# Performance work log

Hardware: AMD Instinct MI355X
Metric: run time of the kernel (lower is better)

## Reference

```python
import jax, jax.numpy as jnp
import numpy as np

EMBED_DIM = 1024
NUM_HEADS = 16
HEAD_DIM = EMBED_DIM // NUM_HEADS


def setup_inputs() -> dict:
    key = jax.random.key(0)
    ks = jax.random.split(key, 9)
    B, T, C = 2, 2048, EMBED_DIM
    s = 1.0 / np.sqrt(C)
    return {
        "x": jax.random.normal(ks[0], (B, T, C), dtype=jnp.float32),
        "Wq": jax.random.normal(ks[1], (C, C), dtype=jnp.float32) * s,
        "bq": jnp.zeros((C,), dtype=jnp.float32),
        "Wk": jax.random.normal(ks[2], (C, C), dtype=jnp.float32) * s,
        "bk": jnp.zeros((C,), dtype=jnp.float32),
        "Wv": jax.random.normal(ks[3], (C, C), dtype=jnp.float32) * s,
        "bv": jnp.zeros((C,), dtype=jnp.float32),
        "Wo": jax.random.normal(ks[4], (C, C), dtype=jnp.float32) * s,
        "bo": jnp.zeros((C,), dtype=jnp.float32),
    }


def reference(x, Wq, bq, Wk, bk, Wv, bv, Wo, bo):
    B, T, C = x.shape
    H, D = NUM_HEADS, HEAD_DIM
    # projections (torch Linear: x @ W.T + b; here W stored as [in,out])
    q = (x @ Wq + bq).reshape(B, T, H, D).transpose(0, 2, 1, 3)  # [B,H,T,D]
    k = (x @ Wk + bk).reshape(B, T, H, D).transpose(0, 2, 1, 3)
    v = (x @ Wv + bv).reshape(B, T, H, D).transpose(0, 2, 1, 3)
    scores = jnp.einsum("bhtd,bhsd->bhts", q, k) / jnp.sqrt(jnp.float32(D))
    causal = jnp.tril(jnp.ones((T, T), dtype=bool))  # keep lower triangle
    scores = jnp.where(causal, scores, -jnp.inf)
    weights = jax.nn.softmax(scores, axis=-1)
    attended = jnp.einsum("bhts,bhsd->bhtd", weights, v)
    attended = attended.transpose(0, 2, 1, 3).reshape(B, T, C)
    return attended @ Wo + bo
```

## Files before the change

kernel.cpp:

```cpp
#include <hip/hip_runtime.h>
#include <math.h>


#define BLOCK 256

typedef __attribute__((ext_vector_type(8))) short bf16x8;
typedef __attribute__((ext_vector_type(4))) float f32x4;
typedef __attribute__((ext_vector_type(16))) float f32x16;

__device__ inline short f2bf(float f) {
  union { float f; unsigned u; } c; c.f = f;
  unsigned u = c.u;
  unsigned r = (u + 0x7fffu + ((u >> 16) & 1u)) >> 16;
  return (short)r;
}

#define GLD_LDS16(g, l)                                            \
  __builtin_amdgcn_global_load_lds(                                \
      (const __attribute__((address_space(1))) unsigned int*)(g),  \
      (__attribute__((address_space(3))) unsigned int*)(l), 16, 0, 0)


__global__ void cvt_x_kernel(const float* __restrict__ x, short* __restrict__ xb) {
  int i = (blockIdx.x * BLOCK + threadIdx.x) * 8;
  float4 a = *(const float4*)(x + i);
  float4 b = *(const float4*)(x + i + 4);
  alignas(16) short o[8];
  o[0] = f2bf(a.x); o[1] = f2bf(a.y); o[2] = f2bf(a.z); o[3] = f2bf(a.w);
  o[4] = f2bf(b.x); o[5] = f2bf(b.y); o[6] = f2bf(b.z); o[7] = f2bf(b.w);
  *(int4*)(xb + i) = *(int4*)o;
}

__global__ void cvt_w_kernel(const float* __restrict__ Wq, const float* __restrict__ Wk,
                             const float* __restrict__ Wv, const float* __restrict__ Wo,
                             short* __restrict__ Wtqkv, short* __restrict__ Wto) {
  __shared__ float tile[32][33];
  int z = blockIdx.z;
  const float* W = (z == 0) ? Wq : (z == 1) ? Wk : (z == 2) ? Wv : Wo;
  short* outp = (z == 3) ? Wto : (Wtqkv + (size_t)z * 1024 * 1024);
  int k0 = blockIdx.x * 32, n0 = blockIdx.y * 32;
  int tr = threadIdx.x >> 5, tc = threadIdx.x & 31;
#pragma unroll
  for (int i = 0; i < 4; i++)
    tile[tr + i * 8][tc] = W[(k0 + tr + i * 8) * 1024 + n0 + tc];
  __syncthreads();
#pragma unroll
  for (int i = 0; i < 4; i++)
    outp[(n0 + tr + i * 8) * 1024 + k0 + tc] = f2bf(tile[tc][tr + i * 8]);
}


__global__ __launch_bounds__(BLOCK) void gemm_qkv_kernel(
    const short* __restrict__ A, const short* __restrict__ Wt,
    const float* __restrict__ bq, const float* __restrict__ bk,
    const float* __restrict__ bv,
    short* __restrict__ Qo, short* __restrict__ Ko, short* __restrict__ Vo) {
  const int Kd = 1024;
  const float QSCL = 0.18033688011f;
  int m0 = blockIdx.x * 128, n0 = blockIdx.y * 128;
  int t = threadIdx.x;
  int lane = t & 63, wv = t >> 6;
  int quad = lane >> 4, lc = lane & 15;
  int wy = wv >> 1, wx = wv & 1;
  __shared__ short As[2][128 * 32];
  __shared__ short Bs[2][128 * 32];
  f32x4 acc[4][4] = {};
  int r0 = t >> 2, c0 = (t & 3) * 8;
  const short* Arow0 = A + (size_t)(m0 + r0) * Kd + c0;
  const short* Arow1 = A + (size_t)(m0 + r0 + 64) * Kd + c0;
  const short* Brow0 = Wt + (size_t)(n0 + r0) * Kd + c0;
  const short* Brow1 = Wt + (size_t)(n0 + r0 + 64) * Kd + c0;
  GLD_LDS16(Arow0, &As[0][8 * t]);
  GLD_LDS16(Arow1, &As[0][8 * t + 2048]);
  GLD_LDS16(Brow0, &Bs[0][8 * t]);
  GLD_LDS16(Brow1, &Bs[0][8 * t + 2048]);
  int cur = 0;
  for (int k0 = 0; k0 < Kd; k0 += 32) {
    __syncthreads();
    if (k0 + 32 < Kd) {
      int nxt = cur ^ 1;
      GLD_LDS16(Arow0 + k0 + 32, &As[nxt][8 * t]);
      GLD_LDS16(Arow1 + k0 + 32, &As[nxt][8 * t + 2048]);
      GLD_LDS16(Brow0 + k0 + 32, &Bs[nxt][8 * t]);
      GLD_LDS16(Brow1 + k0 + 32, &Bs[nxt][8 * t + 2048]);
    }
    bf16x8 af[4], bf[4];
#pragma unroll
    for (int i = 0; i < 4; i++)
      af[i] = *(const bf16x8*)&As[cur][(wy * 64 + i * 16 + lc) * 32 + quad * 8];
#pragma unroll
    for (int i = 0; i < 4; i++)
      bf[i] = *(const bf16x8*)&Bs[cur][(wx * 64 + i * 16 + lc) * 32 + quad * 8];
#pragma unroll
    for (int mi = 0; mi < 4; mi++)
#pragma unroll
      for (int ni = 0; ni < 4; ni++)
        acc[mi][ni] = __builtin_amdgcn_mfma_f32_16x16x32_bf16(af[mi], bf[ni], acc[mi][ni], 0, 0, 0);
    cur ^= 1;
  }
#pragma unroll
  for (int mi = 0; mi < 4; mi++) {
    int row = m0 + wy * 64 + mi * 16 + quad * 4;
#pragma unroll
    for (int ni = 0; ni < 4; ni++) {
      int col = n0 + wx * 64 + ni * 16 + lc;
      int which = col >> 10;
      int hd = col & 1023;
      int h = hd >> 6, d = hd & 63;
      float bb = (which == 0) ? bq[hd] : (which == 1) ? bk[hd] : bv[hd];
      if (which == 2) {
        alignas(8) short pk[4];
#pragma unroll
        for (int r = 0; r < 4; r++) pk[r] = f2bf(acc[mi][ni][r] + bb);
        int b = row >> 11, tt = row & 2047;
        *(int2*)&Vo[((size_t)(b * 16 + h) * 64 + d) * 2048 + tt] = *(const int2*)pk;
      } else {
#pragma unroll
        for (int r = 0; r < 4; r++) {
          int rw = row + r;
          int b = rw >> 11, tt = rw & 2047;
          float val = acc[mi][ni][r] + bb;
          if (which == 0) {
            Qo[((size_t)(b * 16 + h) * 2048 + tt) * 64 + d] = f2bf(val * QSCL);
          } else {
            Ko[((size_t)(b * 16 + h) * 2048 + tt) * 64 + d] = f2bf(val);
          }
        }
      }
    }
  }
}


__global__ __launch_bounds__(BLOCK) void gemm_out_kernel(
    const short* __restrict__ A, const short* __restrict__ Wt,
    const float* __restrict__ bias, float* __restrict__ Out) {
  const int Kd = 1024;
  int m0 = blockIdx.x * 64, n0 = blockIdx.y * 128;
  int t = threadIdx.x;
  int lane = t & 63, wv = t >> 6;
  int quad = lane >> 4, lc = lane & 15;
  int wy = wv >> 1, wx = wv & 1;
  __shared__ short As[64 * 32];
  __shared__ short Bs[128 * 32];
  int r0 = t >> 2, c0 = (t & 3) * 8;
  f32x4 acc[2][4] = {};
  const short* Arow0 = A + (size_t)(m0 + r0) * Kd + c0;
  const short* Brow0 = Wt + (size_t)(n0 + r0) * Kd + c0;
  const short* Brow1 = Wt + (size_t)(n0 + r0 + 64) * Kd + c0;
  for (int k0 = 0; k0 < Kd; k0 += 32) {
    __syncthreads();
    GLD_LDS16(Arow0 + k0, &As[8 * t]);
    GLD_LDS16(Brow0 + k0, &Bs[8 * t]);
    GLD_LDS16(Brow1 + k0, &Bs[8 * t + 2048]);
    __syncthreads();
    bf16x8 af[2], bf[4];
#pragma unroll
    for (int i = 0; i < 2; i++)
      af[i] = *(const bf16x8*)&As[(wy * 32 + i * 16 + lc) * 32 + quad * 8];
#pragma unroll
    for (int i = 0; i < 4; i++)
      bf[i] = *(const bf16x8*)&Bs[(wx * 64 + i * 16 + lc) * 32 + quad * 8];
#pragma unroll
    for (int mi = 0; mi < 2; mi++)
#pragma unroll
      for (int ni = 0; ni < 4; ni++)
        acc[mi][ni] = __builtin_amdgcn_mfma_f32_16x16x32_bf16(af[mi], bf[ni], acc[mi][ni], 0, 0, 0);
  }
#pragma unroll
  for (int mi = 0; mi < 2; mi++) {
    int row = m0 + wy * 32 + mi * 16 + quad * 4;
#pragma unroll
    for (int ni = 0; ni < 4; ni++) {
      int col = n0 + wx * 64 + ni * 16 + lc;
      float bb = bias[col];
#pragma unroll
      for (int r = 0; r < 4; r++)
        Out[(size_t)(row + r) * 1024 + col] = acc[mi][ni][r] + bb;
    }
  }
}


__global__ __launch_bounds__(BLOCK, 3) void attn_kernel(
    const short* __restrict__ Q, const short* __restrict__ K,
    const short* __restrict__ Vt, short* __restrict__ Oa) {
  int bh = blockIdx.x >> 4;
  int pair = blockIdx.x & 15;
  int t = threadIdx.x;
  int lane = t & 63, w = t >> 6;
  int qhalf = w & 1, par = w >> 1;
  int ln = lane & 31, lh = lane >> 5;
  const short* Qb = Q + (size_t)bh * 2048 * 64;
  const short* Kb = K + (size_t)bh * 2048 * 64;
  const short* Vg = Vt + (size_t)bh * 64 * 2048;
  int b = bh >> 4, h = bh & 15;

  __shared__ short Kt[64 * 72];
  __shared__ short Vs[64 * 72];
  __shared__ __align__(16) short Ps[4][32 * 72];
  __shared__ float lx[2][64];
  short* Pw = Ps[w];

  int srow = t >> 2;
  int scol = (t & 3) * 16;
  const float M2 = 14.5f;

  for (int sp = 0; sp < 2; sp++) {
    int s = sp ? (31 - pair) : pair;
    int q0 = s * 64;
    int q0w = q0 + qhalf * 32;
    int ntiles = s + 1;

    bf16x8 qf[4];
#pragma unroll
    for (int c = 0; c < 4; c++)
      qf[c] = *(const bf16x8*)&Qb[(size_t)(q0w + ln) * 64 + c * 16 + lh * 8];

    f32x16 O0 = {}, O1 = {};
    float lsum = 0.f;

    int4 ka0 = *(const int4*)&Kb[(size_t)srow * 64 + scol];
    int4 ka1 = *(const int4*)&Kb[(size_t)srow * 64 + scol + 8];
    int4 va0 = *(const int4*)&Vg[(size_t)srow * 2048 + scol];
    int4 va1 = *(const int4*)&Vg[(size_t)srow * 2048 + scol + 8];
    __syncthreads();
    *(int4*)&Kt[srow * 72 + scol] = ka0;
    *(int4*)&Kt[srow * 72 + scol + 8] = ka1;
    *(int4*)&Vs[srow * 72 + scol] = va0;
    *(int4*)&Vs[srow * 72 + scol + 8] = va1;
    __syncthreads();

    for (int kt = 0; kt < ntiles; kt++) {
      bool more = (kt + 1 < ntiles);
      if (more) {
        int kb2 = (kt + 1) * 64;
        ka0 = *(const int4*)&Kb[(size_t)(kb2 + srow) * 64 + scol];
        ka1 = *(const int4*)&Kb[(size_t)(kb2 + srow) * 64 + scol + 8];
        va0 = *(const int4*)&Vg[(size_t)srow * 2048 + kb2 + scol];
        va1 = *(const int4*)&Vg[(size_t)srow * 2048 + kb2 + scol + 8];
      }
      if ((kt & 1) == par) {
        int kbase = kt * 64;
        f32x16 S[2] = {};
#pragma unroll
        for (int c = 0; c < 4; c++) {
          bf16x8 k0 = *(const bf16x8*)&Kt[ln * 72 + c * 16 + lh * 8];
          bf16x8 k1 = *(const bf16x8*)&Kt[(32 + ln) * 72 + c * 16 + lh * 8];
          S[0] = __builtin_amdgcn_mfma_f32_32x32x16_bf16(k0, qf[c], S[0], 0, 0, 0);
          S[1] = __builtin_amdgcn_mfma_f32_32x32x16_bf16(k1, qf[c], S[1], 0, 0, 0);
        }
        if (kt == ntiles - 1) {
          int qg = q0w + ln;
#pragma unroll
          for (int kh = 0; kh < 2; kh++)
#pragma unroll
            for (int reg = 0; reg < 16; reg++) {
              int key = kbase + kh * 32 + (reg & 3) + 8 * (reg >> 2) + 4 * lh;
              if (key > qg) S[kh][reg] = -3.0e38f;
            }
        }
#pragma unroll
        for (int kh = 0; kh < 2; kh++)
#pragma unroll
          for (int g = 0; g < 4; g++) {
            unsigned u[4];
#pragma unroll
            for (int i = 0; i < 4; i++) {
              union { float f; unsigned v; } cc;
              cc.f = __builtin_amdgcn_exp2f(S[kh][g * 4 + i] - M2);
              lsum += cc.f;
              u[i] = cc.v + 0x8000u;
            }
            int2 pk;
            pk.x = (int)__builtin_amdgcn_perm(u[1], u[0], 0x07060302);
            pk.y = (int)__builtin_amdgcn_perm(u[3], u[2], 0x07060302);
            *(int2*)&Pw[ln * 72 + kh * 32 + g * 8 + lh * 4] = pk;
          }
#pragma unroll
        for (int c = 0; c < 4; c++) {
          bf16x8 pf = *(const bf16x8*)&Pw[ln * 72 + c * 16 + lh * 8];
          bf16x8 v0 = *(const bf16x8*)&Vs[ln * 72 + c * 16 + lh * 8];
          bf16x8 v1 = *(const bf16x8*)&Vs[(32 + ln) * 72 + c * 16 + lh * 8];
          O0 = __builtin_amdgcn_mfma_f32_32x32x16_bf16(v0, pf, O0, 0, 0, 0);
          O1 = __builtin_amdgcn_mfma_f32_32x32x16_bf16(v1, pf, O1, 0, 0, 0);
        }
      }
      if (more) {
        __syncthreads();
        *(int4*)&Kt[srow * 72 + scol] = ka0;
        *(int4*)&Kt[srow * 72 + scol + 8] = ka1;
        *(int4*)&Vs[srow * 72 + scol] = va0;
        *(int4*)&Vs[srow * 72 + scol + 8] = va1;
        __syncthreads();
      }
    }

    float* ob = (float*)&Ps[0][0];
    __syncthreads();
    if (par == 1) {
      float* obw = ob + qhalf * 2048;
#pragma unroll
      for (int dh = 0; dh < 2; dh++)
#pragma unroll
        for (int reg = 0; reg < 16; reg++)
          obw[((dh * 16 + reg) * 2 + lh) * 32 + ln] = dh ? O1[reg] : O0[reg];
      lx[qhalf][lane] = lsum;
    }
    __syncthreads();
    if (par == 0) {
      float* obw = ob + qhalf * 2048;
#pragma unroll
      for (int reg = 0; reg < 16; reg++) {
        O0[reg] += obw[((0 * 16 + reg) * 2 + lh) * 32 + ln];
        O1[reg] += obw[((1 * 16 + reg) * 2 + lh) * 32 + ln];
      }
      float lt = lsum + lx[qhalf][lane];
      lt += __shfl_xor(lt, 32, 64);
      float inv = 1.0f / lt;
      size_t rowbase = (size_t)(b * 2048 + q0w + ln) * 1024 + h * 64;
#pragma unroll
      for (int dh = 0; dh < 2; dh++)
#pragma unroll
        for (int g = 0; g < 4; g++) {
          alignas(8) short pk[4];
#pragma unroll
          for (int i = 0; i < 4; i++) {
            float v = dh ? O1[g * 4 + i] : O0[g * 4 + i];
            pk[i] = f2bf(v * inv);
          }
          *(int2*)&Oa[rowbase + dh * 32 + g * 8 + lh * 4] = *(const int2*)pk;
        }
    }
  }
}


extern "C" void kernel_launch(void* const* d_in, const int* in_sizes, int n_in,
                              void* d_out, int out_size, void* d_ws, size_t ws_size,
                              hipStream_t stream) {
  const float* x = (const float*)d_in[0];
  const float* Wq = (const float*)d_in[1];
  const float* bq = (const float*)d_in[2];
  const float* Wk = (const float*)d_in[3];
  const float* bk = (const float*)d_in[4];
  const float* Wv = (const float*)d_in[5];
  const float* bv = (const float*)d_in[6];
  const float* Wo = (const float*)d_in[7];
  const float* bo = (const float*)d_in[8];
  char* ws = (char*)d_ws;
  const size_t MB = 1024 * 1024;
  short* xb = (short*)(ws);
  short* Wtqkv = (short*)(ws + 8 * MB);
  short* Wto = (short*)(ws + 14 * MB);
  short* Qb = (short*)(ws + 17 * MB);
  short* Kb = (short*)(ws + 25 * MB);
  short* Vb = (short*)(ws + 33 * MB);
  short* Att = (short*)(ws + 41 * MB);
  float* out = (float*)d_out;

  cvt_x_kernel<<<2048, BLOCK, 0, stream>>>(x, xb);
  cvt_w_kernel<<<dim3(32, 32, 4), BLOCK, 0, stream>>>(Wq, Wk, Wv, Wo, Wtqkv, Wto);
  gemm_qkv_kernel<<<dim3(32, 24), BLOCK, 0, stream>>>(xb, Wtqkv, bq, bk, bv, Qb, Kb, Vb);
  attn_kernel<<<512, BLOCK, 0, stream>>>(Qb, Kb, Vb, Att);
  gemm_out_kernel<<<dim3(64, 8), BLOCK, 0, stream>>>(Att, Wto, bo, out);
}
```

Before: 193.5 us.

## Double-buffer output GEMM LDS and restructure attention into 128-key superstages

The output-projection GEMM now double-buffers its LDS tiles with direct global-to-LDS loads, prefetching the next K slice while computing the current one and dropping one barrier per iteration. The attention kernel stages 128 keys per iteration instead of 64 and splits key work between wave pairs by 32-key halves rather than alternating tiles. Key groups lying entirely above the causal diagonal are skipped, and fewer barriers run per key. This uses more LDS and registers, so launch bounds drop from 3 to 2 blocks per CU, which may reduce occupancy.

```diff
diff --git a/kernel.cpp b/kernel.cpp
--- a/kernel.cpp
+++ b/kernel.cpp
@@ -141,31 +141,38 @@
   int lane = t & 63, wv = t >> 6;
   int quad = lane >> 4, lc = lane & 15;
   int wy = wv >> 1, wx = wv & 1;
-  __shared__ short As[64 * 32];
-  __shared__ short Bs[128 * 32];
+  __shared__ short As[2][64 * 32];
+  __shared__ short Bs[2][128 * 32];
   int r0 = t >> 2, c0 = (t & 3) * 8;
   f32x4 acc[2][4] = {};
   const short* Arow0 = A + (size_t)(m0 + r0) * Kd + c0;
   const short* Brow0 = Wt + (size_t)(n0 + r0) * Kd + c0;
   const short* Brow1 = Wt + (size_t)(n0 + r0 + 64) * Kd + c0;
+  GLD_LDS16(Arow0, &As[0][8 * t]);
+  GLD_LDS16(Brow0, &Bs[0][8 * t]);
+  GLD_LDS16(Brow1, &Bs[0][8 * t + 2048]);
+  int cur = 0;
   for (int k0 = 0; k0 < Kd; k0 += 32) {
     __syncthreads();
-    GLD_LDS16(Arow0 + k0, &As[8 * t]);
-    GLD_LDS16(Brow0 + k0, &Bs[8 * t]);
-    GLD_LDS16(Brow1 + k0, &Bs[8 * t + 2048]);
-    __syncthreads();
+    if (k0 + 32 < Kd) {
+      int nxt = cur ^ 1;
+      GLD_LDS16(Arow0 + k0 + 32, &As[nxt][8 * t]);
+      GLD_LDS16(Brow0 + k0 + 32, &Bs[nxt][8 * t]);
+      GLD_LDS16(Brow1 + k0 + 32, &Bs[nxt][8 * t + 2048]);
+    }
     bf16x8 af[2], bf[4];
 #pragma unroll
     for (int i = 0; i < 2; i++)
-      af[i] = *(const bf16x8*)&As[(wy * 32 + i * 16 + lc) * 32 + quad * 8];
+      af[i] = *(const bf16x8*)&As[cur][(wy * 32 + i * 16 + lc) * 32 + quad * 8];
 #pragma unroll
     for (int i = 0; i < 4; i++)
-      bf[i] = *(const bf16x8*)&Bs[(wx * 64 + i * 16 + lc) * 32 + quad * 8];
+      bf[i] = *(const bf16x8*)&Bs[cur][(wx * 64 + i * 16 + lc) * 32 + quad * 8];
 #pragma unroll
     for (int mi = 0; mi < 2; mi++)
 #pragma unroll
       for (int ni = 0; ni < 4; ni++)
         acc[mi][ni] = __builtin_amdgcn_mfma_f32_16x16x32_bf16(af[mi], bf[ni], acc[mi][ni], 0, 0, 0);
+    cur ^= 1;
   }
 #pragma unroll
   for (int mi = 0; mi < 2; mi++) {
@@ -182,35 +189,37 @@
 }
 
 
-__global__ __launch_bounds__(BLOCK, 3) void attn_kernel(
+__global__ __launch_bounds__(BLOCK, 2) void attn_kernel(
     const short* __restrict__ Q, const short* __restrict__ K,
     const short* __restrict__ Vt, short* __restrict__ Oa) {
   int bh = blockIdx.x >> 4;
   int pair = blockIdx.x & 15;
   int t = threadIdx.x;
   int lane = t & 63, w = t >> 6;
-  int qhalf = w & 1, par = w >> 1;
+  int qh = w & 1, kh = w >> 1;
   int ln = lane & 31, lh = lane >> 5;
   const short* Qb = Q + (size_t)bh * 2048 * 64;
   const short* Kb = K + (size_t)bh * 2048 * 64;
   const short* Vg = Vt + (size_t)bh * 64 * 2048;
   int b = bh >> 4, h = bh & 15;
 
-  __shared__ short Kt[64 * 72];
-  __shared__ short Vs[64 * 72];
+  __shared__ short Kt[128 * 72];
+  __shared__ short Vs[64 * 136];
   __shared__ __align__(16) short Ps[4][32 * 72];
   __shared__ float lx[2][64];
   short* Pw = Ps[w];
 
-  int srow = t >> 2;
-  int scol = (t & 3) * 16;
+  int krow = t >> 1, khalf = (t & 1) * 32;
+  int vrow = t >> 2, vq = (t & 3) * 32;
   const float M2 = 14.5f;
 
   for (int sp = 0; sp < 2; sp++) {
     int s = sp ? (31 - pair) : pair;
     int q0 = s * 64;
-    int q0w = q0 + qhalf * 32;
+    int q0w = q0 + qh * 32;
+    int qmax = q0w + 31;
     int ntiles = s + 1;
+    int nss = (ntiles + 1) >> 1;
 
     bf16x8 qf[4];
 #pragma unroll
@@ -220,102 +229,107 @@
     f32x16 O0 = {}, O1 = {};
     float lsum = 0.f;
 
-    int4 ka0 = *(const int4*)&Kb[(size_t)srow * 64 + scol];
-    int4 ka1 = *(const int4*)&Kb[(size_t)srow * 64 + scol + 8];
-    int4 va0 = *(const int4*)&Vg[(size_t)srow * 2048 + scol];
-    int4 va1 = *(const int4*)&Vg[(size_t)srow * 2048 + scol + 8];
-    __syncthreads();
-    *(int4*)&Kt[srow * 72 + scol] = ka0;
-    *(int4*)&Kt[srow * 72 + scol + 8] = ka1;
-    *(int4*)&Vs[srow * 72 + scol] = va0;
-    *(int4*)&Vs[srow * 72 + scol + 8] = va1;
-    __syncthreads();
-
-    for (int kt = 0; kt < ntiles; kt++) {
-      bool more = (kt + 1 < ntiles);
-      if (more) {
-        int kb2 = (kt + 1) * 64;
-        ka0 = *(const int4*)&Kb[(size_t)(kb2 + srow) * 64 + scol];
-        ka1 = *(const int4*)&Kb[(size_t)(kb2 + srow) * 64 + scol + 8];
-        va0 = *(const int4*)&Vg[(size_t)srow * 2048 + kb2 + scol];
-        va1 = *(const int4*)&Vg[(size_t)srow * 2048 + kb2 + scol + 8];
-      }
-      if ((kt & 1) == par) {
-        int kbase = kt * 64;
-        f32x16 S[2] = {};
+    int4 kreg[4], vreg[4];
+#pragma unroll
+    for (int i = 0; i < 4; i++) {
+      kreg[i] = *(const int4*)&Kb[(size_t)krow * 64 + khalf + i * 8];
+      vreg[i] = *(const int4*)&Vg[(size_t)vrow * 2048 + vq + i * 8];
+    }
+    __syncthreads();
+#pragma unroll
+    for (int i = 0; i < 4; i++) {
+      *(int4*)&Kt[krow * 72 + khalf + i * 8] = kreg[i];
+      *(int4*)&Vs[vrow * 136 + vq + i * 8] = vreg[i];
+    }
+    __syncthreads();
+
+    for (int ss = 0; ss < nss; ss++) {
+      if (ss + 1 < nss) {
+        int kb2 = (ss + 1) * 128;
+#pragma unroll
+        for (int i = 0; i < 4; i++) {
+          kreg[i] = *(const int4*)&Kb[(size_t)(kb2 + krow) * 64 + khalf + i * 8];
+          vreg[i] = *(const int4*)&Vg[(size_t)vrow * 2048 + kb2 + vq + i * 8];
+        }
+      }
+      bool gv[2];
+#pragma unroll
+      for (int st = 0; st < 2; st++) {
+        int kt = ss * 2 + st;
+        int grpbase = kt * 64 + kh * 32;
+        gv[st] = (kt < ntiles) && (grpbase <= qmax);
+        if (!gv[st]) continue;
+        f32x16 S = {};
 #pragma unroll
         for (int c = 0; c < 4; c++) {
-          bf16x8 k0 = *(const bf16x8*)&Kt[ln * 72 + c * 16 + lh * 8];
-          bf16x8 k1 = *(const bf16x8*)&Kt[(32 + ln) * 72 + c * 16 + lh * 8];
-          S[0] = __builtin_amdgcn_mfma_f32_32x32x16_bf16(k0, qf[c], S[0], 0, 0, 0);
-          S[1] = __builtin_amdgcn_mfma_f32_32x32x16_bf16(k1, qf[c], S[1], 0, 0, 0);
+          bf16x8 kf = *(const bf16x8*)&Kt[(st * 64 + kh * 32 + ln) * 72 + c * 16 + lh * 8];
+          S = __builtin_amdgcn_mfma_f32_32x32x16_bf16(kf, qf[c], S, 0, 0, 0);
         }
         if (kt == ntiles - 1) {
           int qg = q0w + ln;
 #pragma unroll
-          for (int kh = 0; kh < 2; kh++)
-#pragma unroll
-            for (int reg = 0; reg < 16; reg++) {
-              int key = kbase + kh * 32 + (reg & 3) + 8 * (reg >> 2) + 4 * lh;
-              if (key > qg) S[kh][reg] = -3.0e38f;
-            }
-        }
-#pragma unroll
-        for (int kh = 0; kh < 2; kh++)
-#pragma unroll
-          for (int g = 0; g < 4; g++) {
-            unsigned u[4];
-#pragma unroll
-            for (int i = 0; i < 4; i++) {
-              union { float f; unsigned v; } cc;
-              cc.f = __builtin_amdgcn_exp2f(S[kh][g * 4 + i] - M2);
-              lsum += cc.f;
-              u[i] = cc.v + 0x8000u;
-            }
-            int2 pk;
-            pk.x = (int)__builtin_amdgcn_perm(u[1], u[0], 0x07060302);
-            pk.y = (int)__builtin_amdgcn_perm(u[3], u[2], 0x07060302);
-            *(int2*)&Pw[ln * 72 + kh * 32 + g * 8 + lh * 4] = pk;
+          for (int reg = 0; reg < 16; reg++) {
+            int key = grpbase + (reg & 3) + 8 * (reg >> 2) + 4 * lh;
+            if (key > qg) S[reg] = -3.0e38f;
           }
-#pragma unroll
-        for (int c = 0; c < 4; c++) {
-          bf16x8 pf = *(const bf16x8*)&Pw[ln * 72 + c * 16 + lh * 8];
-          bf16x8 v0 = *(const bf16x8*)&Vs[ln * 72 + c * 16 + lh * 8];
-          bf16x8 v1 = *(const bf16x8*)&Vs[(32 + ln) * 72 + c * 16 + lh * 8];
-          O0 = __builtin_amdgcn_mfma_f32_32x32x16_bf16(v0, pf, O0, 0, 0, 0);
-          O1 = __builtin_amdgcn_mfma_f32_32x32x16_bf16(v1, pf, O1, 0, 0, 0);
-        }
-      }
-      if (more) {
+        }
+#pragma unroll
+        for (int g = 0; g < 4; g++) {
+          unsigned u[4];
+#pragma unroll
+          for (int i = 0; i < 4; i++) {
+            union { float f; unsigned v; } cc;
+            cc.f = __builtin_amdgcn_exp2f(S[g * 4 + i] - M2);
+            lsum += cc.f;
+            u[i] = cc.v + 0x8000u;
+          }
+          int2 pk;
+          pk.x = (int)__builtin_amdgcn_perm(u[1], u[0], 0x07060302);
+          pk.y = (int)__builtin_amdgcn_perm(u[3], u[2], 0x07060302);
+          *(int2*)&Pw[ln * 72 + st * 32 + g * 8 + lh * 4] = pk;
+        }
+      }
+#pragma unroll
+      for (int c = 0; c < 4; c++) {
+        if (!gv[c >> 1]) continue;
+        bf16x8 pf = *(const bf16x8*)&Pw[ln * 72 + c * 16 + lh * 8];
+        int vb = (c >> 1) * 64 + kh * 32 + (c & 1) * 16 + lh * 8;
+        bf16x8 v0 = *(const bf16x8*)&Vs[ln * 136 + vb];
+        bf16x8 v1 = *(const bf16x8*)&Vs[(32 + ln) * 136 + vb];
+        O0 = __builtin_amdgcn_mfma_f32_32x32x16_bf16(v0, pf, O0, 0, 0, 0);
+        O1 = __builtin_amdgcn_mfma_f32_32x32x16_bf16(v1, pf, O1, 0, 0, 0);
+      }
+      if (ss + 1 < nss) {
         __syncthreads();
-        *(int4*)&Kt[srow * 72 + scol] = ka0;
-        *(int4*)&Kt[srow * 72 + scol + 8] = ka1;
-        *(int4*)&Vs[srow * 72 + scol] = va0;
-        *(int4*)&Vs[srow * 72 + scol + 8] = va1;
+#pragma unroll
+        for (int i = 0; i < 4; i++) {
+          *(int4*)&Kt[krow * 72 + khalf + i * 8] = kreg[i];
+          *(int4*)&Vs[vrow * 136 + vq + i * 8] = vreg[i];
+        }
         __syncthreads();
       }
     }
 
     float* ob = (float*)&Ps[0][0];
     __syncthreads();
-    if (par == 1) {
-      float* obw = ob + qhalf * 2048;
+    if (kh == 1) {
+      float* obw = ob + qh * 2048;
 #pragma unroll
       for (int dh = 0; dh < 2; dh++)
 #pragma unroll
         for (int reg = 0; reg < 16; reg++)
           obw[((dh * 16 + reg) * 2 + lh) * 32 + ln] = dh ? O1[reg] : O0[reg];
-      lx[qhalf][lane] = lsum;
-    }
-    __syncthreads();
-    if (par == 0) {
-      float* obw = ob + qhalf * 2048;
+      lx[qh][lane] = lsum;
+    }
+    __syncthreads();
+    if (kh == 0) {
+      float* obw = ob + qh * 2048;
 #pragma unroll
       for (int reg = 0; reg < 16; reg++) {
         O0[reg] += obw[((0 * 16 + reg) * 2 + lh) * 32 + ln];
         O1[reg] += obw[((1 * 16 + reg) * 2 + lh) * 32 + ln];
       }
-      float lt = lsum + lx[qhalf][lane];
+      float lt = lsum + lx[qh][lane];
       lt += __shfl_xor(lt, 32, 64);
       float inv = 1.0f / lt;
       size_t rowbase = (size_t)(b * 2048 + q0w + ln) * 1024 + h * 64;
```

New measurement: 251.2 us. +29.8%, slower.

## Double-buffer output GEMM LDS loads and split attention into smaller 32-query blocks

Applied to the files above, without the earlier changes.

The output-projection GEMM now double-buffers its A and B tiles in LDS, issuing the next tile's global-to-LDS load before computing on the current one, which removes one barrier per k-step. The attention kernel is reorganised to use 128-thread blocks that each handle 32 query rows, giving 1024 blocks instead of 512. Each of the two waves processes its own 32-key half of every 64-key tile, and fully masked halves are skipped. This is meant to improve load balance and occupancy and to cut wasted causal work. The cost is that K/V tiles are loaded by more blocks, so there is more global traffic and staging work per query.

```diff
diff --git a/kernel.cpp b/kernel.cpp
--- a/kernel.cpp
+++ b/kernel.cpp
@@ -141,31 +141,38 @@
   int lane = t & 63, wv = t >> 6;
   int quad = lane >> 4, lc = lane & 15;
   int wy = wv >> 1, wx = wv & 1;
-  __shared__ short As[64 * 32];
-  __shared__ short Bs[128 * 32];
+  __shared__ short As[2][64 * 32];
+  __shared__ short Bs[2][128 * 32];
   int r0 = t >> 2, c0 = (t & 3) * 8;
   f32x4 acc[2][4] = {};
   const short* Arow0 = A + (size_t)(m0 + r0) * Kd + c0;
   const short* Brow0 = Wt + (size_t)(n0 + r0) * Kd + c0;
   const short* Brow1 = Wt + (size_t)(n0 + r0 + 64) * Kd + c0;
+  GLD_LDS16(Arow0, &As[0][8 * t]);
+  GLD_LDS16(Brow0, &Bs[0][8 * t]);
+  GLD_LDS16(Brow1, &Bs[0][8 * t + 2048]);
+  int cur = 0;
   for (int k0 = 0; k0 < Kd; k0 += 32) {
     __syncthreads();
-    GLD_LDS16(Arow0 + k0, &As[8 * t]);
-    GLD_LDS16(Brow0 + k0, &Bs[8 * t]);
-    GLD_LDS16(Brow1 + k0, &Bs[8 * t + 2048]);
-    __syncthreads();
+    if (k0 + 32 < Kd) {
+      int nxt = cur ^ 1;
+      GLD_LDS16(Arow0 + k0 + 32, &As[nxt][8 * t]);
+      GLD_LDS16(Brow0 + k0 + 32, &Bs[nxt][8 * t]);
+      GLD_LDS16(Brow1 + k0 + 32, &Bs[nxt][8 * t + 2048]);
+    }
     bf16x8 af[2], bf[4];
 #pragma unroll
     for (int i = 0; i < 2; i++)
-      af[i] = *(const bf16x8*)&As[(wy * 32 + i * 16 + lc) * 32 + quad * 8];
+      af[i] = *(const bf16x8*)&As[cur][(wy * 32 + i * 16 + lc) * 32 + quad * 8];
 #pragma unroll
     for (int i = 0; i < 4; i++)
-      bf[i] = *(const bf16x8*)&Bs[(wx * 64 + i * 16 + lc) * 32 + quad * 8];
+      bf[i] = *(const bf16x8*)&Bs[cur][(wx * 64 + i * 16 + lc) * 32 + quad * 8];
 #pragma unroll
     for (int mi = 0; mi < 2; mi++)
 #pragma unroll
       for (int ni = 0; ni < 4; ni++)
         acc[mi][ni] = __builtin_amdgcn_mfma_f32_16x16x32_bf16(af[mi], bf[ni], acc[mi][ni], 0, 0, 0);
+    cur ^= 1;
   }
 #pragma unroll
   for (int mi = 0; mi < 2; mi++) {
@@ -182,14 +189,13 @@
 }
 
 
-__global__ __launch_bounds__(BLOCK, 3) void attn_kernel(
+__global__ __launch_bounds__(128, 4) void attn_kernel(
     const short* __restrict__ Q, const short* __restrict__ K,
     const short* __restrict__ Vt, short* __restrict__ Oa) {
-  int bh = blockIdx.x >> 4;
-  int pair = blockIdx.x & 15;
+  int bh = blockIdx.x >> 5;
+  int pair = blockIdx.x & 31;
   int t = threadIdx.x;
   int lane = t & 63, w = t >> 6;
-  int qhalf = w & 1, par = w >> 1;
   int ln = lane & 31, lh = lane >> 5;
   const short* Qb = Q + (size_t)bh * 2048 * 64;
   const short* Kb = K + (size_t)bh * 2048 * 64;
@@ -198,37 +204,45 @@
 
   __shared__ short Kt[64 * 72];
   __shared__ short Vs[64 * 72];
-  __shared__ __align__(16) short Ps[4][32 * 72];
-  __shared__ float lx[2][64];
+  __shared__ __align__(16) short Ps[2][32 * 72];
+  __shared__ float lx[64];
   short* Pw = Ps[w];
 
-  int srow = t >> 2;
-  int scol = (t & 3) * 16;
+  int srow = t >> 1;
+  int scol = (t & 1) * 32;
   const float M2 = 14.5f;
 
   for (int sp = 0; sp < 2; sp++) {
-    int s = sp ? (31 - pair) : pair;
-    int q0 = s * 64;
-    int q0w = q0 + qhalf * 32;
-    int ntiles = s + 1;
+    int s = sp ? (63 - pair) : pair;
+    int q0 = s * 32;
+    int qmax = q0 + 31;
+    int ntiles = (s >> 1) + 1;
 
     bf16x8 qf[4];
 #pragma unroll
     for (int c = 0; c < 4; c++)
-      qf[c] = *(const bf16x8*)&Qb[(size_t)(q0w + ln) * 64 + c * 16 + lh * 8];
+      qf[c] = *(const bf16x8*)&Qb[(size_t)(q0 + ln) * 64 + c * 16 + lh * 8];
 
     f32x16 O0 = {}, O1 = {};
     float lsum = 0.f;
 
     int4 ka0 = *(const int4*)&Kb[(size_t)srow * 64 + scol];
     int4 ka1 = *(const int4*)&Kb[(size_t)srow * 64 + scol + 8];
+    int4 ka2 = *(const int4*)&Kb[(size_t)srow * 64 + scol + 16];
+    int4 ka3 = *(const int4*)&Kb[(size_t)srow * 64 + scol + 24];
     int4 va0 = *(const int4*)&Vg[(size_t)srow * 2048 + scol];
     int4 va1 = *(const int4*)&Vg[(size_t)srow * 2048 + scol + 8];
+    int4 va2 = *(const int4*)&Vg[(size_t)srow * 2048 + scol + 16];
+    int4 va3 = *(const int4*)&Vg[(size_t)srow * 2048 + scol + 24];
     __syncthreads();
     *(int4*)&Kt[srow * 72 + scol] = ka0;
     *(int4*)&Kt[srow * 72 + scol + 8] = ka1;
+    *(int4*)&Kt[srow * 72 + scol + 16] = ka2;
+    *(int4*)&Kt[srow * 72 + scol + 24] = ka3;
     *(int4*)&Vs[srow * 72 + scol] = va0;
     *(int4*)&Vs[srow * 72 + scol + 8] = va1;
+    *(int4*)&Vs[srow * 72 + scol + 16] = va2;
+    *(int4*)&Vs[srow * 72 + scol + 24] = va3;
     __syncthreads();
 
     for (int kt = 0; kt < ntiles; kt++) {
@@ -237,51 +251,50 @@
         int kb2 = (kt + 1) * 64;
         ka0 = *(const int4*)&Kb[(size_t)(kb2 + srow) * 64 + scol];
         ka1 = *(const int4*)&Kb[(size_t)(kb2 + srow) * 64 + scol + 8];
+        ka2 = *(const int4*)&Kb[(size_t)(kb2 + srow) * 64 + scol + 16];
+        ka3 = *(const int4*)&Kb[(size_t)(kb2 + srow) * 64 + scol + 24];
         va0 = *(const int4*)&Vg[(size_t)srow * 2048 + kb2 + scol];
         va1 = *(const int4*)&Vg[(size_t)srow * 2048 + kb2 + scol + 8];
-      }
-      if ((kt & 1) == par) {
-        int kbase = kt * 64;
-        f32x16 S[2] = {};
+        va2 = *(const int4*)&Vg[(size_t)srow * 2048 + kb2 + scol + 16];
+        va3 = *(const int4*)&Vg[(size_t)srow * 2048 + kb2 + scol + 24];
+      }
+      int grpbase = kt * 64 + w * 32;
+      if (grpbase <= qmax) {
+        f32x16 S = {};
 #pragma unroll
         for (int c = 0; c < 4; c++) {
-          bf16x8 k0 = *(const bf16x8*)&Kt[ln * 72 + c * 16 + lh * 8];
-          bf16x8 k1 = *(const bf16x8*)&Kt[(32 + ln) * 72 + c * 16 + lh * 8];
-          S[0] = __builtin_amdgcn_mfma_f32_32x32x16_bf16(k0, qf[c], S[0], 0, 0, 0);
-          S[1] = __builtin_amdgcn_mfma_f32_32x32x16_bf16(k1, qf[c], S[1], 0, 0, 0);
+          bf16x8 kf = *(const bf16x8*)&Kt[(w * 32 + ln) * 72 + c * 16 + lh * 8];
+          S = __builtin_amdgcn_mfma_f32_32x32x16_bf16(kf, qf[c], S, 0, 0, 0);
         }
         if (kt == ntiles - 1) {
-          int qg = q0w + ln;
-#pragma unroll
-          for (int kh = 0; kh < 2; kh++)
-#pragma unroll
-            for (int reg = 0; reg < 16; reg++) {
-              int key = kbase + kh * 32 + (reg & 3) + 8 * (reg >> 2) + 4 * lh;
-              if (key > qg) S[kh][reg] = -3.0e38f;
-            }
-        }
-#pragma unroll
-        for (int kh = 0; kh < 2; kh++)
-#pragma unroll
-          for (int g = 0; g < 4; g++) {
-            unsigned u[4];
-#pragma unroll
-            for (int i = 0; i < 4; i++) {
-              union { float f; unsigned v; } cc;
-              cc.f = __builtin_amdgcn_exp2f(S[kh][g * 4 + i] - M2);
-              lsum += cc.f;
-              u[i] = cc.v + 0x8000u;
-            }
-            int2 pk;
-            pk.x = (int)__builtin_amdgcn_perm(u[1], u[0], 0x07060302);
-            pk.y = (int)__builtin_amdgcn_perm(u[3], u[2], 0x07060302);
-            *(int2*)&Pw[ln * 72 + kh * 32 + g * 8 + lh * 4] = pk;
+          int qg = q0 + ln;
+#pragma unroll
+          for (int reg = 0; reg < 16; reg++) {
+            int key = grpbase + (reg & 3) + 8 * (reg >> 2) + 4 * lh;
+            if (key > qg) S[reg] = -3.0e38f;
           }
-#pragma unroll
-        for (int c = 0; c < 4; c++) {
-          bf16x8 pf = *(const bf16x8*)&Pw[ln * 72 + c * 16 + lh * 8];
-          bf16x8 v0 = *(const bf16x8*)&Vs[ln * 72 + c * 16 + lh * 8];
-          bf16x8 v1 = *(const bf16x8*)&Vs[(32 + ln) * 72 + c * 16 + lh * 8];
+        }
+#pragma unroll
+        for (int g = 0; g < 4; g++) {
+          unsigned u[4];
+#pragma unroll
+          for (int i = 0; i < 4; i++) {
+            union { float f; unsigned v; } cc;
+            cc.f = __builtin_amdgcn_exp2f(S[g * 4 + i] - M2);
+            lsum += cc.f;
+            u[i] = cc.v + 0x8000u;
+          }
+          int2 pk;
+          pk.x = (int)__builtin_amdgcn_perm(u[1], u[0], 0x07060302);
+          pk.y = (int)__builtin_amdgcn_perm(u[3], u[2], 0x07060302);
+          *(int2*)&Pw[ln * 72 + g * 8 + lh * 4] = pk;
+        }
+#pragma unroll
+        for (int c2 = 0; c2 < 2; c2++) {
+          bf16x8 pf = *(const bf16x8*)&Pw[ln * 72 + c2 * 16 + lh * 8];
+          int vb = w * 32 + c2 * 16 + lh * 8;
+          bf16x8 v0 = *(const bf16x8*)&Vs[ln * 72 + vb];
+          bf16x8 v1 = *(const bf16x8*)&Vs[(32 + ln) * 72 + vb];
           O0 = __builtin_amdgcn_mfma_f32_32x32x16_bf16(v0, pf, O0, 0, 0, 0);
           O1 = __builtin_amdgcn_mfma_f32_32x32x16_bf16(v1, pf, O1, 0, 0, 0);
         }
@@ -290,35 +303,37 @@
         __syncthreads();
         *(int4*)&Kt[srow * 72 + scol] = ka0;
         *(int4*)&Kt[srow * 72 + scol + 8] = ka1;
+        *(int4*)&Kt[srow * 72 + scol + 16] = ka2;
+        *(int4*)&Kt[srow * 72 + scol + 24] = ka3;
         *(int4*)&Vs[srow * 72 + scol] = va0;
         *(int4*)&Vs[srow * 72 + scol + 8] = va1;
+        *(int4*)&Vs[srow * 72 + scol + 16] = va2;
+        *(int4*)&Vs[srow * 72 + scol + 24] = va3;
         __syncthreads();
       }
     }
 
     float* ob = (float*)&Ps[0][0];
     __syncthreads();
-    if (par == 1) {
-      float* obw = ob + qhalf * 2048;
+    if (w == 1) {
 #pragma unroll
       for (int dh = 0; dh < 2; dh++)
 #pragma unroll
         for (int reg = 0; reg < 16; reg++)
-          obw[((dh * 16 + reg) * 2 + lh) * 32 + ln] = dh ? O1[reg] : O0[reg];
-      lx[qhalf][lane] = lsum;
-    }
-    __syncthreads();
-    if (par == 0) {
-      float* obw = ob + qhalf * 2048;
+          ob[((dh * 16 + reg) * 2 + lh) * 32 + ln] = dh ? O1[reg] : O0[reg];
+      lx[lane] = lsum;
+    }
+    __syncthreads();
+    if (w == 0) {
 #pragma unroll
       for (int reg = 0; reg < 16; reg++) {
-        O0[reg] += obw[((0 * 16 + reg) * 2 + lh) * 32 + ln];
-        O1[reg] += obw[((1 * 16 + reg) * 2 + lh) * 32 + ln];
-      }
-      float lt = lsum + lx[qhalf][lane];
+        O0[reg] += ob[((0 * 16 + reg) * 2 + lh) * 32 + ln];
+        O1[reg] += ob[((1 * 16 + reg) * 2 + lh) * 32 + ln];
+      }
+      float lt = lsum + lx[lane];
       lt += __shfl_xor(lt, 32, 64);
       float inv = 1.0f / lt;
-      size_t rowbase = (size_t)(b * 2048 + q0w + ln) * 1024 + h * 64;
+      size_t rowbase = (size_t)(b * 2048 + q0 + ln) * 1024 + h * 64;
 #pragma unroll
       for (int dh = 0; dh < 2; dh++)
 #pragma unroll
@@ -332,6 +347,7 @@
           *(int2*)&Oa[rowbase + dh * 32 + g * 8 + lh * 4] = *(const int2*)pk;
         }
     }
+    __syncthreads();
   }
 }
 
@@ -362,6 +378,6 @@
   cvt_x_kernel<<<2048, BLOCK, 0, stream>>>(x, xb);
   cvt_w_kernel<<<dim3(32, 32, 4), BLOCK, 0, stream>>>(Wq, Wk, Wv, Wo, Wtqkv, Wto);
   gemm_qkv_kernel<<<dim3(32, 24), BLOCK, 0, stream>>>(xb, Wtqkv, bq, bk, bv, Qb, Kb, Vb);
-  attn_kernel<<<512, BLOCK, 0, stream>>>(Qb, Kb, Vb, Att);
+  attn_kernel<<<1024, 128, 0, stream>>>(Qb, Kb, Vb, Att);
   gemm_out_kernel<<<dim3(64, 8), BLOCK, 0, stream>>>(Att, Wto, bo, out);
 }
```

New measurement: 216.7 us. 12.0% more time.
